# Performance work log

Measured on AMD Instinct MI355X. Metric: run time of the kernel, lower is better.

The kernel has to match this reference:

```python
import jax, jax.numpy as jnp
import numpy as np

DIM = 64
KSZ = 3


def _conv2d(x, w, b):
    # x: (N, C, H, W), w: (O, I, 3, 3), 'same' padding
    y = jax.lax.conv_general_dilated(
        x, w, window_strides=(1, 1), padding=[(1, 1), (1, 1)],
        dimension_numbers=("NCHW", "OIHW", "NCHW"))
    return y + b[None, :, None, None]


def setup_inputs() -> dict:
    key = jax.random.key(0)
    k1, k2, k3, k4, k5 = jax.random.split(key, 5)
    b, c, t, h, w = 2, DIM, 5, 128, 128
    x = jax.random.normal(k1, (b, c, t, h, w), dtype=jnp.float32)
    # Conv3d kernels have temporal extent 1 -> equivalent 2D kernels
    w1 = jax.random.normal(k2, (DIM, DIM, 3, 3), dtype=jnp.float32) * 0.05
    b1 = jax.random.normal(k3, (DIM,), dtype=jnp.float32) * 0.05
    w2 = jax.random.normal(k4, (KSZ * KSZ, DIM, 3, 3), dtype=jnp.float32) * 0.05
    b2 = jax.random.normal(k5, (KSZ * KSZ,), dtype=jnp.float32) * 0.05
    return {"x": x, "w1": w1, "b1": b1, "w2": w2, "b2": b2}


def reference(x, w1, b1, w2, b2):
    b, c, t, h, w = x.shape
    k = KSZ
    K = t * k * k
    # Conv3d with (1,3,3) kernel == 2D conv applied per frame
    xf = x.transpose(0, 2, 1, 3, 4).reshape(b * t, c, h, w)  # (bt, c, h, w)
    y = _conv2d(xf, w1, b1)
    y = jnp.where(y >= 0, y, 0.2 * y)  # LeakyReLU(0.2)
    ker = _conv2d(y, w2, b2)  # (bt, k*k, h, w)
    # rearrange 'b (k1 k2) t h w -> b h w (t k1 k2)'
    ker = ker.reshape(b, t, k * k, h, w).transpose(0, 3, 4, 1, 2).reshape(b, h, w, K)
    ker = ker[:, None]  # (b, 1, h, w, K)
    # kernel_normalize over last dim
    ker = ker - jnp.mean(ker, axis=-1, keepdims=True) + 1.0 / K
    # replicate pad + unfold (gather kxk neighborhoods)
    pad = (k - 1) // 2
    xp = jnp.pad(xf, ((0, 0), (0, 0), (pad, pad), (pad, pad)), mode="edge")
    patches = jnp.stack(
        [xp[:, :, i:i + h, j:j + w] for i in range(k) for j in range(k)],
        axis=-1)  # (bt, c, h, w, k*k) in (k1,k2) order like F.unfold
    # '(b t) (c k1 k2) (h w) -> b c h w (t k1 k2)'
    patches = patches.reshape(b, t, c, h, w, k * k).transpose(0, 2, 3, 4, 1, 5)
    patches = patches.reshape(b, c, h, w, K)
    return jnp.sum(patches * ker, axis=-1)  # (b, c, h, w)
```

## Files before the change

### kernel.cpp

```cpp
#include <hip/hip_runtime.h>
#include <hip/hip_bf16.h>

#define HH 128
#define WW 128
#define CC 64
#define TT 5
#define HW (HH*WW)
#define NI 10

typedef __attribute__((ext_vector_type(8))) short short8;
typedef __attribute__((ext_vector_type(4))) float f32x4;

typedef const unsigned int __attribute__((address_space(1))) gu32;
typedef unsigned int __attribute__((address_space(3))) lu32;

__device__ __forceinline__ void gl_lds16(const void* g, void* l) {
  __builtin_amdgcn_global_load_lds((gu32*)g, (lu32*)l, 16, 0, 0);
}

__device__ __forceinline__ float bf2f(unsigned int bits16) {
  union { unsigned int u; float f; } v; v.u = bits16 << 16; return v.f;
}
__device__ __forceinline__ unsigned short f2bf(float f) {
  __hip_bfloat16 h = __float2bfloat16(f);
  return *reinterpret_cast<unsigned short*>(&h);
}


__global__ __launch_bounds__(256) void pack_k(const float* __restrict__ x,
    const float* __restrict__ w1, const float* __restrict__ w2,
    unsigned short* __restrict__ xb, unsigned short* __restrict__ wb1,
    unsigned short* __restrict__ wb2) {
  __shared__ unsigned short tb[128*68];
  const int tid = threadIdx.x;
  const int bx = blockIdx.x;
  if (bx >= NI*HH) {
    int idx = (bx - NI*HH)*256 + tid;
    if (idx < 64*576) {
      int oc = idx / 576, rem = idx - oc*576, kk = rem >> 6, ic = rem & 63;
      wb1[idx] = f2bf(w1[(oc*64 + ic)*9 + kk]);
    }
    if (idx < 16*576) {
      int oc = idx / 576, rem = idx - oc*576, kk = rem >> 6, ic = rem & 63;
      wb2[idx] = (oc < 9) ? f2bf(w2[(oc*64 + ic)*9 + kk]) : (unsigned short)0;
    }
    return;
  }
  const int n = bx >> 7, h = bx & 127;
  const int bi = n / 5, ti = n - bi*5;
  const float* xp = x + ((size_t)bi*CC*TT + ti)*HW + (size_t)h*WW;
  for (int e = tid; e < 64*128; e += 256) {
    int ci = e >> 7, w = e & 127;
    tb[w*68 + ci] = f2bf(xp[(size_t)ci*TT*HW + w]);
  }
  __syncthreads();
  for (int e = tid; e < 1024; e += 256) {
    int w = e >> 3, cg = e & 7;
    uint2 lo = *(const uint2*)(&tb[w*68 + cg*8]);
    uint2 hi = *(const uint2*)(&tb[w*68 + cg*8 + 4]);
    uint4 v; v.x = lo.x; v.y = lo.y; v.z = hi.x; v.w = hi.y;
    *(uint4*)(xb + (((size_t)(n*8 + cg))*HW + (size_t)h*WW + w)*8) = v;
  }
}

__global__ __launch_bounds__(256, 2) void conv1_mfma(
    const unsigned short* __restrict__ xb, const unsigned short* __restrict__ wb1,
    const float* __restrict__ b1, unsigned short* __restrict__ yb) {
  __shared__ unsigned short xt[324*64];
  __shared__ unsigned short wt[36*512];
  const int tid = threadIdx.x;
  const int wave = tid >> 6, lane = tid & 63, q = lane >> 4, r = lane & 15;
  const int n = blockIdx.z;
  const int h0 = blockIdx.y << 4, w0 = blockIdx.x << 4;
  const int wbase = tid & ~63;

  {
    #pragma unroll
    for (int it = 0; it < 9; ++it) {
      int e = tid + it*256;
      int frag = e >> 6, ln = e & 63;
      int kk = frag >> 2, rem = frag & 3, half = rem >> 1, g = rem & 1;
      const unsigned short* src = wb1 + (size_t)(g*16 + (ln & 15))*576
                                  + kk*64 + half*32 + ((ln >> 4) << 3);
      gl_lds16(src, (char*)wt + ((size_t)(it*256 + wbase) << 4));
    }
  }
  const bool interior = (blockIdx.x >= 1) & (blockIdx.x <= 6) &
                        (blockIdx.y >= 1) & (blockIdx.y <= 6);
  if (interior) {
    #pragma unroll
    for (int it = 0; it < 11; ++it) {
      int e = tid + it*256;
      if (e < 2592) {
        int sp = e >> 3, c = e & 7;
        int cs = c ^ (sp & 7);
        int sr = sp / 18, sc = sp - sr*18;
        int gh = h0 + sr - 1, gw = w0 + sc - 1;
        const unsigned short* src = xb + (((size_t)(n*8 + cs))*HW + gh*WW + gw)*8;
        gl_lds16(src, (char*)xt + ((size_t)(it*256 + wbase) << 4));
      }
    }
  } else {
    for (int e = tid; e < 2592; e += 256) {
      int sp = e >> 3, c = e & 7;
      int sr = sp / 18, sc = sp - sr*18;
      int gh = h0 + sr - 1, gw = w0 + sc - 1;
      uint4 v = make_uint4(0u,0u,0u,0u);
      if (gh >= 0 && gh < HH && gw >= 0 && gw < WW)
        v = *(const uint4*)(xb + (((size_t)(n*8 + c))*HW + gh*WW + gw)*8);
      *(uint4*)(&xt[sp*64 + ((c ^ (sp & 7)) << 3)]) = v;
    }
  }
  __syncthreads();

  f32x4 zero4 = {0.f, 0.f, 0.f, 0.f};

  #pragma unroll
  for (int g2 = 0; g2 < 2; ++g2) {
    f32x4 acc[4][2];
    #pragma unroll
    for (int i = 0; i < 4; ++i)
      #pragma unroll
      for (int g = 0; g < 2; ++g) acc[i][g] = zero4;

    #pragma unroll
    for (int half = 0; half < 2; ++half) {
      short8 bf[6][3];
      #pragma unroll
      for (int rr = 0; rr < 6; ++rr)
        #pragma unroll
        for (int dx = 0; dx < 3; ++dx) {
          int sp = (wave*4 + rr)*18 + (r + dx);
          bf[rr][dx] = *(const short8*)(&xt[sp*64 + ((((half << 2) | q) ^ (sp & 7)) << 3)]);
        }
      #pragma unroll
      for (int kk = 0; kk < 9; ++kk) {
        const int dy = kk / 3, dx = kk - dy*3;
        short8 a0 = *(const short8*)(&wt[((kk*4 + half*2 + 0) << 9) + (lane << 3)]);
        short8 a1 = *(const short8*)(&wt[((kk*4 + half*2 + 1) << 9) + (lane << 3)]);
        #pragma unroll
        for (int i = 0; i < 4; ++i) {
          acc[i][0] = __builtin_amdgcn_mfma_f32_16x16x32_bf16(a0, bf[i+dy][dx], acc[i][0], 0, 0, 0);
          acc[i][1] = __builtin_amdgcn_mfma_f32_16x16x32_bf16(a1, bf[i+dy][dx], acc[i][1], 0, 0, 0);
        }
      }
    }

    if (g2 == 0) {
      __syncthreads();
      #pragma unroll
      for (int it = 0; it < 9; ++it) {
        int e = tid + it*256;
        int frag = e >> 6, ln = e & 63;
        int kk = frag >> 2, rem = frag & 3, half = rem >> 1, g = rem & 1;
        const unsigned short* src = wb1 + (size_t)(32 + g*16 + (ln & 15))*576
                                    + kk*64 + half*32 + ((ln >> 4) << 3);
        gl_lds16(src, (char*)wt + ((size_t)(it*256 + wbase) << 4));
      }
    }

    #pragma unroll
    for (int i = 0; i < 4; ++i) {
      int py = wave*4 + i;
      unsigned short* yp = yb + ((size_t)n*HW + (h0+py)*WW + (w0+r))*64;
      #pragma unroll
      for (int g = 0; g < 2; ++g) {
        int oc0 = (g2 << 5) + g*16 + (q << 2);
        f32x4 bias = *(const f32x4*)(b1 + oc0);
        float v0 = acc[i][g][0] + bias[0]; v0 = (v0 >= 0.f) ? v0 : 0.2f*v0;
        float v1 = acc[i][g][1] + bias[1]; v1 = (v1 >= 0.f) ? v1 : 0.2f*v1;
        float v2 = acc[i][g][2] + bias[2]; v2 = (v2 >= 0.f) ? v2 : 0.2f*v2;
        float v3 = acc[i][g][3] + bias[3]; v3 = (v3 >= 0.f) ? v3 : 0.2f*v3;
        uint2 pk;
        pk.x = (unsigned int)f2bf(v0) | ((unsigned int)f2bf(v1) << 16);
        pk.y = (unsigned int)f2bf(v2) | ((unsigned int)f2bf(v3) << 16);
        *(uint2*)(yp + oc0) = pk;
      }
    }

    if (g2 == 0) __syncthreads();
  }
}

__global__ __launch_bounds__(256) void conv2_mfma(
    const unsigned short* __restrict__ yb, const unsigned short* __restrict__ wb2,
    const float* __restrict__ b2, float* __restrict__ ker0) {
  __shared__ unsigned short yt[180*64];
  __shared__ unsigned short wt[18*512];
  const int tid = threadIdx.x;
  const int wave = tid >> 6, lane = tid & 63, q = lane >> 4, r = lane & 15;
  const int n = blockIdx.z;
  const int h0 = blockIdx.y << 3, w0 = blockIdx.x << 4;
  const unsigned short* yn = yb + (size_t)n*HW*64;
  const int wbase = tid & ~63;

  #pragma unroll
  for (int it = 0; it < 5; ++it) {
    int e = tid + it*256;
    if (e < 1152) {
      int frag = e >> 6, ln = e & 63;
      int kk = frag >> 1, half = frag & 1;
      const unsigned short* src = wb2 + (size_t)(ln & 15)*576 + kk*64
                                  + half*32 + ((ln >> 4) << 3);
      gl_lds16(src, (char*)wt + ((size_t)(it*256 + wbase) << 4));
    }
  }
  const bool interior = (blockIdx.x >= 1) & (blockIdx.x <= 6) &
                        (blockIdx.y >= 1) & (blockIdx.y <= 14);
  if (interior) {
    #pragma unroll
    for (int it = 0; it < 6; ++it) {
      int e = tid + it*256;
      if (e < 1440) {
        int sp = e >> 3, c = e & 7;
        int cs = c ^ (sp & 7);
        int sr = sp / 18, sc = sp - sr*18;
        int gh = h0 + sr - 1, gw = w0 + sc - 1;
        const unsigned short* src = yn + ((size_t)(gh*WW + gw))*64 + (cs << 3);
        gl_lds16(src, (char*)yt + ((size_t)(it*256 + wbase) << 4));
      }
    }
  } else {
    for (int e = tid; e < 1440; e += 256) {
      int sp = e >> 3, c = e & 7;
      int sr = sp / 18, sc = sp - sr*18;
      int gh = h0 + sr - 1, gw = w0 + sc - 1;
      uint4 v = make_uint4(0u,0u,0u,0u);
      if (gh >= 0 && gh < HH && gw >= 0 && gw < WW)
        v = *(const uint4*)(yn + ((size_t)(gh*WW + gw))*64 + (c << 3));
      *(uint4*)(&yt[sp*64 + ((c ^ (sp & 7)) << 3)]) = v;
    }
  }
  __syncthreads();

  f32x4 zero4 = {0.f, 0.f, 0.f, 0.f};
  f32x4 acc[2];
  #pragma unroll
  for (int i = 0; i < 2; ++i) acc[i] = zero4;

  #pragma unroll
  for (int half = 0; half < 2; ++half) {
    short8 bf[4][3];
    #pragma unroll
    for (int rr = 0; rr < 4; ++rr)
      #pragma unroll
      for (int dx = 0; dx < 3; ++dx) {
        int sp = (wave*2 + rr)*18 + (r + dx);
        bf[rr][dx] = *(const short8*)(&yt[sp*64 + ((((half << 2) | q) ^ (sp & 7)) << 3)]);
      }
    #pragma unroll
    for (int kk = 0; kk < 9; ++kk) {
      const int dy = kk / 3, dx = kk - dy*3;
      short8 a = *(const short8*)(&wt[((kk*2 + half) << 9) + (lane << 3)]);
      #pragma unroll
      for (int i = 0; i < 2; ++i)
        acc[i] = __builtin_amdgcn_mfma_f32_16x16x32_bf16(a, bf[i+dy][dx], acc[i], 0, 0, 0);
    }
  }

  #pragma unroll
  for (int i = 0; i < 2; ++i) {
    int py = wave*2 + i;
    #pragma unroll
    for (int t2 = 0; t2 < 4; ++t2) {
      int oc = (q << 2) + t2;
      if (oc < 9)
        ker0[((size_t)n*9 + oc)*HW + (h0+py)*WW + w0 + r] = acc[i][t2] + b2[oc];
    }
  }
}

__global__ __launch_bounds__(256) void dynf_k(
    const unsigned short* __restrict__ xb, const float* __restrict__ ker0,
    float* __restrict__ out) {
  __shared__ float xs0[TT*324*4];
  __shared__ float xs1[TT*324*4];
  const int tw = threadIdx.x, th = threadIdx.y;
  const int tid = th*16 + tw;
  const int wz = blockIdx.z;
  const int bi = wz >> 2, cio = (wz & 3) << 4;
  const int h0 = blockIdx.y << 4, w0 = blockIdx.x << 4;
  const int pix = (h0+th)*WW + w0 + tw;

  float kv[45]; float s = 0.f;
  #pragma unroll
  for (int t5 = 0; t5 < TT; ++t5)
    #pragma unroll
    for (int kk = 0; kk < 9; ++kk) {
      float v = ker0[((size_t)(bi*TT + t5)*9 + kk)*HW + pix];
      kv[t5*9 + kk] = v; s += v;
    }
  const float m = (s - 1.f) * (1.f/45.f);
  #pragma unroll
  for (int qq = 0; qq < 45; ++qq) kv[qq] -= m;

  for (int co = 0; co < 2; ++co) {
    const int ci0 = cio + (co << 3);
    const int cg = ci0 >> 3;
    __syncthreads();
    for (int e = tid; e < TT*324; e += 256) {
      int t5 = e / 324, sp = e - t5*324;
      int rr = sp / 18, cc = sp - rr*18;
      int gh = min(max(h0 + rr - 1, 0), HH-1);
      int gw = min(max(w0 + cc - 1, 0), WW-1);
      uint4 raw = *(const uint4*)(xb + (((size_t)((bi*TT + t5)*8 + cg))*HW + gh*WW + gw)*8);
      xs0[(e << 2) + 0] = bf2f(raw.x & 0xffffu);
      xs0[(e << 2) + 1] = bf2f(raw.x >> 16);
      xs0[(e << 2) + 2] = bf2f(raw.y & 0xffffu);
      xs0[(e << 2) + 3] = bf2f(raw.y >> 16);
      xs1[(e << 2) + 0] = bf2f(raw.z & 0xffffu);
      xs1[(e << 2) + 1] = bf2f(raw.z >> 16);
      xs1[(e << 2) + 2] = bf2f(raw.w & 0xffffu);
      xs1[(e << 2) + 3] = bf2f(raw.w >> 16);
    }
    __syncthreads();

    #pragma unroll
    for (int p = 0; p < 2; ++p) {
      const float* plane = p ? xs1 : xs0;
      float a0 = 0.f, a1 = 0.f, a2 = 0.f, a3 = 0.f;
      #pragma unroll
      for (int t5 = 0; t5 < TT; ++t5)
        #pragma unroll
        for (int dy = 0; dy < 3; ++dy)
          #pragma unroll
          for (int dx = 0; dx < 3; ++dx) {
            f32x4 xv = *(const f32x4*)(&plane[(t5*324 + (th+dy)*18 + (tw+dx)) << 2]);
            float k = kv[t5*9 + dy*3 + dx];
            a0 = fmaf(xv[0], k, a0); a1 = fmaf(xv[1], k, a1);
            a2 = fmaf(xv[2], k, a2); a3 = fmaf(xv[3], k, a3);
          }
      float* op = out + ((size_t)(bi*CC + ci0 + p*4))*HW + pix;
      op[0] = a0; op[HW] = a1; op[2*(size_t)HW] = a2; op[3*(size_t)HW] = a3;
    }
  }
}

extern "C" void kernel_launch(void* const* d_in, const int* in_sizes, int n_in,
                              void* d_out, int out_size, void* d_ws, size_t ws_size,
                              hipStream_t stream) {
  const float* x  = (const float*)d_in[0];
  const float* w1 = (const float*)d_in[1];
  const float* b1 = (const float*)d_in[2];
  const float* w2 = (const float*)d_in[3];
  const float* b2 = (const float*)d_in[4];
  float* out = (float*)d_out;

  unsigned short* xb  = (unsigned short*)d_ws;
  unsigned short* yb  = xb + (size_t)NI*HW*64;
  float*          ker0 = (float*)(yb + (size_t)NI*HW*64);
  unsigned short* wb1 = (unsigned short*)(ker0 + (size_t)NI*9*HW);
  unsigned short* wb2 = wb1 + 64*576;

  pack_k    <<<NI*HH + 144, 256, 0, stream>>>(x, w1, w2, xb, wb1, wb2);
  conv1_mfma<<<dim3(8,8,NI), 256, 0, stream>>>(xb, wb1, b1, yb);
  conv2_mfma<<<dim3(8,16,NI), 256, 0, stream>>>(yb, wb2, b2, ker0);
  dynf_k    <<<dim3(8,8,8), dim3(16,16), 0, stream>>>(xb, ker0, out);
}
```

Baseline: 143.9 us.

## Fuse four stage kernels into one cooperative persistent kernel with grid syncs

Merges pack, conv1, conv2 and dynamic-filter stages into a single cooperative mega-kernel launched with 512 blocks, looping over work items per stage and separating stages with grid.sync(). This removes three kernel launch boundaries and their drain/ramp gaps. It falls back to the original four launches if the cooperative launch fails. The trade-offs are a fixed grid size, grid-wide barrier costs, and a larger shared allocation (78 KB) that may limit occupancy to 2 blocks per CU.

```diff
diff --git a/kernel.cpp b/kernel.cpp
--- a/kernel.cpp
+++ b/kernel.cpp
@@ -1,5 +1,8 @@
 #include <hip/hip_runtime.h>
+#include <hip/hip_cooperative_groups.h>
 #include <hip/hip_bf16.h>
+
+namespace cg = cooperative_groups;
 
 #define HH 128
 #define WW 128
@@ -26,6 +29,326 @@
   return *reinterpret_cast<unsigned short*>(&h);
 }
 
+
+__global__ __launch_bounds__(256, 2) void mega_k(
+    const float* __restrict__ x, const float* __restrict__ w1,
+    const float* __restrict__ b1, const float* __restrict__ w2,
+    const float* __restrict__ b2,
+    unsigned short* __restrict__ xb, unsigned short* __restrict__ yb,
+    float* __restrict__ ker0, unsigned short* __restrict__ wb1,
+    unsigned short* __restrict__ wb2, float* __restrict__ out) {
+  __shared__ __align__(64) char smem[78336];
+  const int tid = threadIdx.x;
+  const int nb = gridDim.x;
+  cg::grid_group grid = cg::this_grid();
+
+  {
+    unsigned short* tb = (unsigned short*)smem;
+    for (int bx = blockIdx.x; bx < NI*HH + 144; bx += nb) {
+      if (bx >= NI*HH) {
+        int idx = (bx - NI*HH)*256 + tid;
+        if (idx < 64*576) {
+          int oc = idx / 576, rem = idx - oc*576, kk = rem >> 6, ic = rem & 63;
+          wb1[idx] = f2bf(w1[(oc*64 + ic)*9 + kk]);
+        }
+        if (idx < 16*576) {
+          int oc = idx / 576, rem = idx - oc*576, kk = rem >> 6, ic = rem & 63;
+          wb2[idx] = (oc < 9) ? f2bf(w2[(oc*64 + ic)*9 + kk]) : (unsigned short)0;
+        }
+      } else {
+        const int n = bx >> 7, h = bx & 127;
+        const int bi = n / 5, ti = n - bi*5;
+        const float* xp = x + ((size_t)bi*CC*TT + ti)*HW + (size_t)h*WW;
+        for (int e = tid; e < 64*128; e += 256) {
+          int ci = e >> 7, w = e & 127;
+          tb[w*68 + ci] = f2bf(xp[(size_t)ci*TT*HW + w]);
+        }
+        __syncthreads();
+        for (int e = tid; e < 1024; e += 256) {
+          int w = e >> 3, cgp = e & 7;
+          uint2 lo = *(const uint2*)(&tb[w*68 + cgp*8]);
+          uint2 hi = *(const uint2*)(&tb[w*68 + cgp*8 + 4]);
+          uint4 v; v.x = lo.x; v.y = lo.y; v.z = hi.x; v.w = hi.y;
+          *(uint4*)(xb + (((size_t)(n*8 + cgp))*HW + (size_t)h*WW + w)*8) = v;
+        }
+        __syncthreads();
+      }
+    }
+  }
+  grid.sync();
+
+  {
+    unsigned short* xt = (unsigned short*)smem;
+    unsigned short* wt = (unsigned short*)(smem + 41472);
+    const int wave = tid >> 6, lane = tid & 63, q = lane >> 4, r = lane & 15;
+    const int wbase = tid & ~63;
+
+    for (int item = blockIdx.x; item < 640; item += nb) {
+      const int bxi = item & 7, byi = (item >> 3) & 7, n = item >> 6;
+      const int h0 = byi << 4, w0 = bxi << 4;
+
+      #pragma unroll
+      for (int it = 0; it < 9; ++it) {
+        int e = tid + it*256;
+        int frag = e >> 6, ln = e & 63;
+        int kk = frag >> 2, rem = frag & 3, half = rem >> 1, g = rem & 1;
+        const unsigned short* src = wb1 + (size_t)(g*16 + (ln & 15))*576
+                                    + kk*64 + half*32 + ((ln >> 4) << 3);
+        gl_lds16(src, (char*)wt + ((size_t)(it*256 + wbase) << 4));
+      }
+      const bool interior = (bxi >= 1) & (bxi <= 6) & (byi >= 1) & (byi <= 6);
+      if (interior) {
+        #pragma unroll
+        for (int it = 0; it < 11; ++it) {
+          int e = tid + it*256;
+          if (e < 2592) {
+            int sp = e >> 3, c = e & 7;
+            int cs = c ^ (sp & 7);
+            int sr = sp / 18, sc = sp - sr*18;
+            int gh = h0 + sr - 1, gw = w0 + sc - 1;
+            const unsigned short* src = xb + (((size_t)(n*8 + cs))*HW + gh*WW + gw)*8;
+            gl_lds16(src, (char*)xt + ((size_t)(it*256 + wbase) << 4));
+          }
+        }
+      } else {
+        for (int e = tid; e < 2592; e += 256) {
+          int sp = e >> 3, c = e & 7;
+          int sr = sp / 18, sc = sp - sr*18;
+          int gh = h0 + sr - 1, gw = w0 + sc - 1;
+          uint4 v = make_uint4(0u,0u,0u,0u);
+          if (gh >= 0 && gh < HH && gw >= 0 && gw < WW)
+            v = *(const uint4*)(xb + (((size_t)(n*8 + c))*HW + gh*WW + gw)*8);
+          *(uint4*)(&xt[sp*64 + ((c ^ (sp & 7)) << 3)]) = v;
+        }
+      }
+      __syncthreads();
+
+      f32x4 zero4 = {0.f, 0.f, 0.f, 0.f};
+      #pragma unroll
+      for (int g2 = 0; g2 < 2; ++g2) {
+        f32x4 acc[4][2];
+        #pragma unroll
+        for (int i = 0; i < 4; ++i)
+          #pragma unroll
+          for (int g = 0; g < 2; ++g) acc[i][g] = zero4;
+
+        #pragma unroll
+        for (int half = 0; half < 2; ++half) {
+          short8 bf[6][3];
+          #pragma unroll
+          for (int rr = 0; rr < 6; ++rr)
+            #pragma unroll
+            for (int dx = 0; dx < 3; ++dx) {
+              int sp = (wave*4 + rr)*18 + (r + dx);
+              bf[rr][dx] = *(const short8*)(&xt[sp*64 + ((((half << 2) | q) ^ (sp & 7)) << 3)]);
+            }
+          #pragma unroll
+          for (int kk = 0; kk < 9; ++kk) {
+            const int dy = kk / 3, dx = kk - dy*3;
+            short8 a0 = *(const short8*)(&wt[((kk*4 + half*2 + 0) << 9) + (lane << 3)]);
+            short8 a1 = *(const short8*)(&wt[((kk*4 + half*2 + 1) << 9) + (lane << 3)]);
+            #pragma unroll
+            for (int i = 0; i < 4; ++i) {
+              acc[i][0] = __builtin_amdgcn_mfma_f32_16x16x32_bf16(a0, bf[i+dy][dx], acc[i][0], 0, 0, 0);
+              acc[i][1] = __builtin_amdgcn_mfma_f32_16x16x32_bf16(a1, bf[i+dy][dx], acc[i][1], 0, 0, 0);
+            }
+          }
+        }
+
+        if (g2 == 0) {
+          __syncthreads();
+          #pragma unroll
+          for (int it = 0; it < 9; ++it) {
+            int e = tid + it*256;
+            int frag = e >> 6, ln = e & 63;
+            int kk = frag >> 2, rem = frag & 3, half = rem >> 1, g = rem & 1;
+            const unsigned short* src = wb1 + (size_t)(32 + g*16 + (ln & 15))*576
+                                        + kk*64 + half*32 + ((ln >> 4) << 3);
+            gl_lds16(src, (char*)wt + ((size_t)(it*256 + wbase) << 4));
+          }
+        }
+
+        #pragma unroll
+        for (int i = 0; i < 4; ++i) {
+          int py = wave*4 + i;
+          unsigned short* yp = yb + ((size_t)n*HW + (h0+py)*WW + (w0+r))*64;
+          #pragma unroll
+          for (int g = 0; g < 2; ++g) {
+            int oc0 = (g2 << 5) + g*16 + (q << 2);
+            f32x4 bias = *(const f32x4*)(b1 + oc0);
+            float v0 = acc[i][g][0] + bias[0]; v0 = (v0 >= 0.f) ? v0 : 0.2f*v0;
+            float v1 = acc[i][g][1] + bias[1]; v1 = (v1 >= 0.f) ? v1 : 0.2f*v1;
+            float v2 = acc[i][g][2] + bias[2]; v2 = (v2 >= 0.f) ? v2 : 0.2f*v2;
+            float v3 = acc[i][g][3] + bias[3]; v3 = (v3 >= 0.f) ? v3 : 0.2f*v3;
+            uint2 pk;
+            pk.x = (unsigned int)f2bf(v0) | ((unsigned int)f2bf(v1) << 16);
+            pk.y = (unsigned int)f2bf(v2) | ((unsigned int)f2bf(v3) << 16);
+            *(uint2*)(yp + oc0) = pk;
+          }
+        }
+
+        if (g2 == 0) __syncthreads();
+      }
+      __syncthreads();
+    }
+  }
+  grid.sync();
+
+  {
+    unsigned short* yt = (unsigned short*)smem;
+    unsigned short* wt = (unsigned short*)(smem + 23040);
+    const int wave = tid >> 6, lane = tid & 63, q = lane >> 4, r = lane & 15;
+    const int wbase = tid & ~63;
+
+    for (int item = blockIdx.x; item < 1280; item += nb) {
+      const int bxi = item & 7, byi = (item >> 3) & 15, n = item >> 7;
+      const int h0 = byi << 3, w0 = bxi << 4;
+      const unsigned short* yn = yb + (size_t)n*HW*64;
+
+      #pragma unroll
+      for (int it = 0; it < 5; ++it) {
+        int e = tid + it*256;
+        if (e < 1152) {
+          int frag = e >> 6, ln = e & 63;
+          int kk = frag >> 1, half = frag & 1;
+          const unsigned short* src = wb2 + (size_t)(ln & 15)*576 + kk*64
+                                      + half*32 + ((ln >> 4) << 3);
+          gl_lds16(src, (char*)wt + ((size_t)(it*256 + wbase) << 4));
+        }
+      }
+      const bool interior = (bxi >= 1) & (bxi <= 6) & (byi >= 1) & (byi <= 14);
+      if (interior) {
+        #pragma unroll
+        for (int it = 0; it < 6; ++it) {
+          int e = tid + it*256;
+          if (e < 1440) {
+            int sp = e >> 3, c = e & 7;
+            int cs = c ^ (sp & 7);
+            int sr = sp / 18, sc = sp - sr*18;
+            int gh = h0 + sr - 1, gw = w0 + sc - 1;
+            const unsigned short* src = yn + ((size_t)(gh*WW + gw))*64 + (cs << 3);
+            gl_lds16(src, (char*)yt + ((size_t)(it*256 + wbase) << 4));
+          }
+        }
+      } else {
+        for (int e = tid; e < 1440; e += 256) {
+          int sp = e >> 3, c = e & 7;
+          int sr = sp / 18, sc = sp - sr*18;
+          int gh = h0 + sr - 1, gw = w0 + sc - 1;
+          uint4 v = make_uint4(0u,0u,0u,0u);
+          if (gh >= 0 && gh < HH && gw >= 0 && gw < WW)
+            v = *(const uint4*)(yn + ((size_t)(gh*WW + gw))*64 + (c << 3));
+          *(uint4*)(&yt[sp*64 + ((c ^ (sp & 7)) << 3)]) = v;
+        }
+      }
+      __syncthreads();
+
+      f32x4 zero4 = {0.f, 0.f, 0.f, 0.f};
+      f32x4 acc[2];
+      #pragma unroll
+      for (int i = 0; i < 2; ++i) acc[i] = zero4;
+
+      #pragma unroll
+      for (int half = 0; half < 2; ++half) {
+        short8 bf[4][3];
+        #pragma unroll
+        for (int rr = 0; rr < 4; ++rr)
+          #pragma unroll
+          for (int dx = 0; dx < 3; ++dx) {
+            int sp = (wave*2 + rr)*18 + (r + dx);
+            bf[rr][dx] = *(const short8*)(&yt[sp*64 + ((((half << 2) | q) ^ (sp & 7)) << 3)]);
+          }
+        #pragma unroll
+        for (int kk = 0; kk < 9; ++kk) {
+          const int dy = kk / 3, dx = kk - dy*3;
+          short8 a = *(const short8*)(&wt[((kk*2 + half) << 9) + (lane << 3)]);
+          #pragma unroll
+          for (int i = 0; i < 2; ++i)
+            acc[i] = __builtin_amdgcn_mfma_f32_16x16x32_bf16(a, bf[i+dy][dx], acc[i], 0, 0, 0);
+        }
+      }
+
+      #pragma unroll
+      for (int i = 0; i < 2; ++i) {
+        int py = wave*2 + i;
+        #pragma unroll
+        for (int t2 = 0; t2 < 4; ++t2) {
+          int oc = (q << 2) + t2;
+          if (oc < 9)
+            ker0[((size_t)n*9 + oc)*HW + (h0+py)*WW + w0 + r] = acc[i][t2] + b2[oc];
+        }
+      }
+      __syncthreads();
+    }
+  }
+  grid.sync();
+
+  {
+    float* xs0 = (float*)smem;
+    float* xs1 = (float*)(smem + 25920);
+    const int tw = tid & 15, th = tid >> 4;
+
+    for (int item = blockIdx.x; item < 512; item += nb) {
+      const int bxi = item & 7, byi = (item >> 3) & 7, wz = item >> 6;
+      const int bi = wz >> 2, cio = (wz & 3) << 4;
+      const int h0 = byi << 4, w0 = bxi << 4;
+      const int pix = (h0+th)*WW + w0 + tw;
+
+      float kv[45]; float s = 0.f;
+      #pragma unroll
+      for (int t5 = 0; t5 < TT; ++t5)
+        #pragma unroll
+        for (int kk = 0; kk < 9; ++kk) {
+          float v = ker0[((size_t)(bi*TT + t5)*9 + kk)*HW + pix];
+          kv[t5*9 + kk] = v; s += v;
+        }
+      const float m = (s - 1.f) * (1.f/45.f);
+      #pragma unroll
+      for (int qq = 0; qq < 45; ++qq) kv[qq] -= m;
+
+      for (int co = 0; co < 2; ++co) {
+        const int ci0 = cio + (co << 3);
+        const int cgp = ci0 >> 3;
+        __syncthreads();
+        for (int e = tid; e < TT*324; e += 256) {
+          int t5 = e / 324, sp = e - t5*324;
+          int rr = sp / 18, cc = sp - rr*18;
+          int gh = min(max(h0 + rr - 1, 0), HH-1);
+          int gw = min(max(w0 + cc - 1, 0), WW-1);
+          uint4 raw = *(const uint4*)(xb + (((size_t)((bi*TT + t5)*8 + cgp))*HW + gh*WW + gw)*8);
+          xs0[(e << 2) + 0] = bf2f(raw.x & 0xffffu);
+          xs0[(e << 2) + 1] = bf2f(raw.x >> 16);
+          xs0[(e << 2) + 2] = bf2f(raw.y & 0xffffu);
+          xs0[(e << 2) + 3] = bf2f(raw.y >> 16);
+          xs1[(e << 2) + 0] = bf2f(raw.z & 0xffffu);
+          xs1[(e << 2) + 1] = bf2f(raw.z >> 16);
+          xs1[(e << 2) + 2] = bf2f(raw.w & 0xffffu);
+          xs1[(e << 2) + 3] = bf2f(raw.w >> 16);
+        }
+        __syncthreads();
+
+        #pragma unroll
+        for (int p = 0; p < 2; ++p) {
+          const float* plane = p ? xs1 : xs0;
+          float a0 = 0.f, a1 = 0.f, a2 = 0.f, a3 = 0.f;
+          #pragma unroll
+          for (int t5 = 0; t5 < TT; ++t5)
+            #pragma unroll
+            for (int dy = 0; dy < 3; ++dy)
+              #pragma unroll
+              for (int dx = 0; dx < 3; ++dx) {
+                f32x4 xv = *(const f32x4*)(&plane[(t5*324 + (th+dy)*18 + (tw+dx)) << 2]);
+                float k = kv[t5*9 + dy*3 + dx];
+                a0 = fmaf(xv[0], k, a0); a1 = fmaf(xv[1], k, a1);
+                a2 = fmaf(xv[2], k, a2); a3 = fmaf(xv[3], k, a3);
+              }
+          float* op = out + ((size_t)(bi*CC + ci0 + p*4))*HW + pix;
+          op[0] = a0; op[HW] = a1; op[2*(size_t)HW] = a2; op[3*(size_t)HW] = a3;
+        }
+      }
+    }
+  }
+}
 
 __global__ __launch_bounds__(256) void pack_k(const float* __restrict__ x,
     const float* __restrict__ w1, const float* __restrict__ w2,
@@ -55,11 +378,11 @@
   }
   __syncthreads();
   for (int e = tid; e < 1024; e += 256) {
-    int w = e >> 3, cg = e & 7;
-    uint2 lo = *(const uint2*)(&tb[w*68 + cg*8]);
-    uint2 hi = *(const uint2*)(&tb[w*68 + cg*8 + 4]);
+    int w = e >> 3, cgp = e & 7;
+    uint2 lo = *(const uint2*)(&tb[w*68 + cgp*8]);
+    uint2 hi = *(const uint2*)(&tb[w*68 + cgp*8 + 4]);
     uint4 v; v.x = lo.x; v.y = lo.y; v.z = hi.x; v.w = hi.y;
-    *(uint4*)(xb + (((size_t)(n*8 + cg))*HW + (size_t)h*WW + w)*8) = v;
+    *(uint4*)(xb + (((size_t)(n*8 + cgp))*HW + (size_t)h*WW + w)*8) = v;
   }
 }
 
@@ -73,17 +396,14 @@
   const int n = blockIdx.z;
   const int h0 = blockIdx.y << 4, w0 = blockIdx.x << 4;
   const int wbase = tid & ~63;
-
-  {
-    #pragma unroll
-    for (int it = 0; it < 9; ++it) {
-      int e = tid + it*256;
-      int frag = e >> 6, ln = e & 63;
-      int kk = frag >> 2, rem = frag & 3, half = rem >> 1, g = rem & 1;
-      const unsigned short* src = wb1 + (size_t)(g*16 + (ln & 15))*576
-                                  + kk*64 + half*32 + ((ln >> 4) << 3);
-      gl_lds16(src, (char*)wt + ((size_t)(it*256 + wbase) << 4));
-    }
+  #pragma unroll
+  for (int it = 0; it < 9; ++it) {
+    int e = tid + it*256;
+    int frag = e >> 6, ln = e & 63;
+    int kk = frag >> 2, rem = frag & 3, half = rem >> 1, g = rem & 1;
+    const unsigned short* src = wb1 + (size_t)(g*16 + (ln & 15))*576
+                                + kk*64 + half*32 + ((ln >> 4) << 3);
+    gl_lds16(src, (char*)wt + ((size_t)(it*256 + wbase) << 4));
   }
   const bool interior = (blockIdx.x >= 1) & (blockIdx.x <= 6) &
                         (blockIdx.y >= 1) & (blockIdx.y <= 6);
@@ -112,9 +432,7 @@
     }
   }
   __syncthreads();
-
   f32x4 zero4 = {0.f, 0.f, 0.f, 0.f};
-
   #pragma unroll
   for (int g2 = 0; g2 < 2; ++g2) {
     f32x4 acc[4][2];
@@ -122,7 +440,6 @@
     for (int i = 0; i < 4; ++i)
       #pragma unroll
       for (int g = 0; g < 2; ++g) acc[i][g] = zero4;
-
     #pragma unroll
     for (int half = 0; half < 2; ++half) {
       short8 bf[6][3];
@@ -145,7 +462,6 @@
         }
       }
     }
-
     if (g2 == 0) {
       __syncthreads();
       #pragma unroll
@@ -158,7 +474,6 @@
         gl_lds16(src, (char*)wt + ((size_t)(it*256 + wbase) << 4));
       }
     }
-
     #pragma unroll
     for (int i = 0; i < 4; ++i) {
       int py = wave*4 + i;
@@ -177,7 +492,6 @@
         *(uint2*)(yp + oc0) = pk;
       }
     }
-
     if (g2 == 0) __syncthreads();
   }
 }
@@ -193,7 +507,6 @@
   const int h0 = blockIdx.y << 3, w0 = blockIdx.x << 4;
   const unsigned short* yn = yb + (size_t)n*HW*64;
   const int wbase = tid & ~63;
-
   #pragma unroll
   for (int it = 0; it < 5; ++it) {
     int e = tid + it*256;
@@ -232,12 +545,10 @@
     }
   }
   __syncthreads();
-
   f32x4 zero4 = {0.f, 0.f, 0.f, 0.f};
   f32x4 acc[2];
   #pragma unroll
   for (int i = 0; i < 2; ++i) acc[i] = zero4;
-
   #pragma unroll
   for (int half = 0; half < 2; ++half) {
     short8 bf[4][3];
@@ -257,7 +568,6 @@
         acc[i] = __builtin_amdgcn_mfma_f32_16x16x32_bf16(a, bf[i+dy][dx], acc[i], 0, 0, 0);
     }
   }
-
   #pragma unroll
   for (int i = 0; i < 2; ++i) {
     int py = wave*2 + i;
@@ -281,7 +591,6 @@
   const int bi = wz >> 2, cio = (wz & 3) << 4;
   const int h0 = blockIdx.y << 4, w0 = blockIdx.x << 4;
   const int pix = (h0+th)*WW + w0 + tw;
-
   float kv[45]; float s = 0.f;
   #pragma unroll
   for (int t5 = 0; t5 < TT; ++t5)
@@ -293,17 +602,16 @@
   const float m = (s - 1.f) * (1.f/45.f);
   #pragma unroll
   for (int qq = 0; qq < 45; ++qq) kv[qq] -= m;
-
   for (int co = 0; co < 2; ++co) {
     const int ci0 = cio + (co << 3);
-    const int cg = ci0 >> 3;
+    const int cgp = ci0 >> 3;
     __syncthreads();
     for (int e = tid; e < TT*324; e += 256) {
       int t5 = e / 324, sp = e - t5*324;
       int rr = sp / 18, cc = sp - rr*18;
       int gh = min(max(h0 + rr - 1, 0), HH-1);
       int gw = min(max(w0 + cc - 1, 0), WW-1);
-      uint4 raw = *(const uint4*)(xb + (((size_t)((bi*TT + t5)*8 + cg))*HW + gh*WW + gw)*8);
+      uint4 raw = *(const uint4*)(xb + (((size_t)((bi*TT + t5)*8 + cgp))*HW + gh*WW + gw)*8);
       xs0[(e << 2) + 0] = bf2f(raw.x & 0xffffu);
       xs0[(e << 2) + 1] = bf2f(raw.x >> 16);
       xs0[(e << 2) + 2] = bf2f(raw.y & 0xffffu);
@@ -314,7 +622,6 @@
       xs1[(e << 2) + 3] = bf2f(raw.w >> 16);
     }
     __syncthreads();
-
     #pragma unroll
     for (int p = 0; p < 2; ++p) {
       const float* plane = p ? xs1 : xs0;
@@ -352,8 +659,15 @@
   unsigned short* wb1 = (unsigned short*)(ker0 + (size_t)NI*9*HW);
   unsigned short* wb2 = wb1 + 64*576;
 
-  pack_k    <<<NI*HH + 144, 256, 0, stream>>>(x, w1, w2, xb, wb1, wb2);
-  conv1_mfma<<<dim3(8,8,NI), 256, 0, stream>>>(xb, wb1, b1, yb);
-  conv2_mfma<<<dim3(8,16,NI), 256, 0, stream>>>(yb, wb2, b2, ker0);
-  dynf_k    <<<dim3(8,8,8), dim3(16,16), 0, stream>>>(xb, ker0, out);
-}
+  void* args[] = { (void*)&x, (void*)&w1, (void*)&b1, (void*)&w2, (void*)&b2,
+                   (void*)&xb, (void*)&yb, (void*)&ker0, (void*)&wb1,
+                   (void*)&wb2, (void*)&out };
+  hipError_t err = hipLaunchCooperativeKernel((const void*)mega_k,
+      dim3(512), dim3(256), args, 0, stream);
+  if (err != hipSuccess) {
+    pack_k    <<<NI*HH + 144, 256, 0, stream>>>(x, w1, w2, xb, wb1, wb2);
+    conv1_mfma<<<dim3(8,8,NI), 256, 0, stream>>>(xb, wb1, b1, yb);
+    conv2_mfma<<<dim3(8,16,NI), 256, 0, stream>>>(yb, wb2, b2, ker0);
+    dynf_k    <<<dim3(8,8,8), dim3(16,16), 0, stream>>>(xb, ker0, out);
+  }
+}
```

Result: slower. 346.1 us (+140.5%).

## Load conv1 input fragments directly from global memory instead of LDS tile

Applied to the files above, without the earlier changes.

Removes the shared-memory staging of the 18x18x64 bf16 input halo in conv1 and has each lane read its MFMA B fragments straight from global memory, with zero-fill on border tiles. Dropping the ~41KB input LDS buffer lets launch bounds rise from 2 to 3 blocks per CU. The trade-off is redundant global/L2 reads: each input pixel is now fetched by several lanes and again for the second output-channel half (g2), and the loads are no longer asynchronous global-to-LDS copies.

```diff
diff --git a/kernel.cpp b/kernel.cpp
--- a/kernel.cpp
+++ b/kernel.cpp
@@ -63,54 +63,31 @@
   }
 }
 
-__global__ __launch_bounds__(256, 2) void conv1_mfma(
+#define STAGE_W1(OCBASE) do {                                               \
+    _Pragma("unroll")                                                       \
+    for (int it = 0; it < 9; ++it) {                                        \
+      int e = tid + it*256;                                                 \
+      int frag = e >> 6, ln = e & 63;                                       \
+      int kk = frag >> 2, rem = frag & 3, half = rem >> 1, g = rem & 1;     \
+      const unsigned short* src = wb1 + (size_t)((OCBASE) + g*16 + (ln & 15))*576 \
+                                  + kk*64 + half*32 + ((ln >> 4) << 3);     \
+      gl_lds16(src, (char*)wt + ((size_t)(it*256 + wbase) << 4));           \
+    }                                                                       \
+  } while (0)
+
+__global__ __launch_bounds__(256, 3) void conv1_mfma(
     const unsigned short* __restrict__ xb, const unsigned short* __restrict__ wb1,
     const float* __restrict__ b1, unsigned short* __restrict__ yb) {
-  __shared__ unsigned short xt[324*64];
   __shared__ unsigned short wt[36*512];
   const int tid = threadIdx.x;
   const int wave = tid >> 6, lane = tid & 63, q = lane >> 4, r = lane & 15;
   const int n = blockIdx.z;
   const int h0 = blockIdx.y << 4, w0 = blockIdx.x << 4;
   const int wbase = tid & ~63;
-
-  {
-    #pragma unroll
-    for (int it = 0; it < 9; ++it) {
-      int e = tid + it*256;
-      int frag = e >> 6, ln = e & 63;
-      int kk = frag >> 2, rem = frag & 3, half = rem >> 1, g = rem & 1;
-      const unsigned short* src = wb1 + (size_t)(g*16 + (ln & 15))*576
-                                  + kk*64 + half*32 + ((ln >> 4) << 3);
-      gl_lds16(src, (char*)wt + ((size_t)(it*256 + wbase) << 4));
-    }
-  }
   const bool interior = (blockIdx.x >= 1) & (blockIdx.x <= 6) &
                         (blockIdx.y >= 1) & (blockIdx.y <= 6);
-  if (interior) {
-    #pragma unroll
-    for (int it = 0; it < 11; ++it) {
-      int e = tid + it*256;
-      if (e < 2592) {
-        int sp = e >> 3, c = e & 7;
-        int cs = c ^ (sp & 7);
-        int sr = sp / 18, sc = sp - sr*18;
-        int gh = h0 + sr - 1, gw = w0 + sc - 1;
-        const unsigned short* src = xb + (((size_t)(n*8 + cs))*HW + gh*WW + gw)*8;
-        gl_lds16(src, (char*)xt + ((size_t)(it*256 + wbase) << 4));
-      }
-    }
-  } else {
-    for (int e = tid; e < 2592; e += 256) {
-      int sp = e >> 3, c = e & 7;
-      int sr = sp / 18, sc = sp - sr*18;
-      int gh = h0 + sr - 1, gw = w0 + sc - 1;
-      uint4 v = make_uint4(0u,0u,0u,0u);
-      if (gh >= 0 && gh < HH && gw >= 0 && gw < WW)
-        v = *(const uint4*)(xb + (((size_t)(n*8 + c))*HW + gh*WW + gw)*8);
-      *(uint4*)(&xt[sp*64 + ((c ^ (sp & 7)) << 3)]) = v;
-    }
-  }
+
+  STAGE_W1(0);
   __syncthreads();
 
   f32x4 zero4 = {0.f, 0.f, 0.f, 0.f};
@@ -126,13 +103,36 @@
     #pragma unroll
     for (int half = 0; half < 2; ++half) {
       short8 bf[6][3];
-      #pragma unroll
-      for (int rr = 0; rr < 6; ++rr)
+      if (interior) {
         #pragma unroll
-        for (int dx = 0; dx < 3; ++dx) {
-          int sp = (wave*4 + rr)*18 + (r + dx);
-          bf[rr][dx] = *(const short8*)(&xt[sp*64 + ((((half << 2) | q) ^ (sp & 7)) << 3)]);
+        for (int rr = 0; rr < 6; ++rr) {
+          const int gh = h0 + (wave << 2) + rr - 1;
+          #pragma unroll
+          for (int dx = 0; dx < 3; ++dx) {
+            const int gw = w0 + r + dx - 1;
+            const int cg = (half << 2) | q;
+            bf[rr][dx] = *(const short8*)(xb +
+                (((size_t)((n << 3) + cg))*HW + gh*WW + gw)*8);
+          }
         }
+      } else {
+        #pragma unroll
+        for (int rr = 0; rr < 6; ++rr) {
+          const int gh = h0 + (wave << 2) + rr - 1;
+          #pragma unroll
+          for (int dx = 0; dx < 3; ++dx) {
+            const int gw = w0 + r + dx - 1;
+            const int cg = (half << 2) | q;
+            const bool ok = ((unsigned)gh < (unsigned)HH) &
+                            ((unsigned)gw < (unsigned)WW);
+            const size_t off = ok ? (size_t)(gh*WW + gw) : (size_t)0;
+            uint4 v = *(const uint4*)(xb +
+                (((size_t)((n << 3) + cg))*HW + off)*8);
+            if (!ok) v = make_uint4(0u, 0u, 0u, 0u);
+            bf[rr][dx] = *reinterpret_cast<short8*>(&v);
+          }
+        }
+      }
       #pragma unroll
       for (int kk = 0; kk < 9; ++kk) {
         const int dy = kk / 3, dx = kk - dy*3;
@@ -148,15 +148,7 @@
 
     if (g2 == 0) {
       __syncthreads();
-      #pragma unroll
-      for (int it = 0; it < 9; ++it) {
-        int e = tid + it*256;
-        int frag = e >> 6, ln = e & 63;
-        int kk = frag >> 2, rem = frag & 3, half = rem >> 1, g = rem & 1;
-        const unsigned short* src = wb1 + (size_t)(32 + g*16 + (ln & 15))*576
-                                    + kk*64 + half*32 + ((ln >> 4) << 3);
-        gl_lds16(src, (char*)wt + ((size_t)(it*256 + wbase) << 4));
-      }
+      STAGE_W1(32);
     }
 
     #pragma unroll
```

New measurement: 143.2 us. No clear change (-0.5%).
